# Kernel optimization log

Measured on AMD Instinct MI355X. Metric: run time of the kernel, lower is better.

Reference implementation:

```python
import jax, jax.numpy as jnp
import numpy as np

N_NODES = 50000
N_EDGES = 500000
D_IN = 128
D_HID = 128
OUTPUT_DIM = 10.0


def gcn_conv(x, src, dst, edge_weight, W, b, n_nodes):
    # PyG GCNConv: out = D^{-1/2} (A + I) D^{-1/2} X W + b, self-loop weight 1
    xw = x @ W  # [N, D_out]
    # degree at target nodes, including self-loop weight 1
    deg = jax.ops.segment_sum(edge_weight, dst, num_segments=n_nodes) + 1.0
    dinv = jnp.where(deg > 0, jax.lax.rsqrt(deg), 0.0)  # [N]
    norm = dinv[src] * edge_weight * dinv[dst]  # [E]
    msgs = xw[src] * norm[:, None]  # [E, D_out] gathered+scaled messages
    agg = jax.ops.segment_sum(msgs, dst, num_segments=n_nodes)
    # analytic self-loop contribution: norm_ii = dinv_i * 1 * dinv_i
    agg = agg + xw * (dinv * dinv)[:, None]
    return agg + b


def setup_inputs() -> dict:
    key = jax.random.key(0)
    k = jax.random.split(key, 8)
    x = jax.random.normal(k[0], (N_NODES, D_IN), dtype=jnp.float32)
    edge_index = jax.random.randint(k[1], (2, N_EDGES), 0, N_NODES, dtype=jnp.int64)
    edge_weight = jax.random.uniform(k[2], (N_EDGES,), dtype=jnp.float32)
    s1 = 1.0 / np.sqrt(D_IN)
    s2 = 1.0 / np.sqrt(D_HID)
    W1 = jax.random.uniform(k[3], (D_IN, D_HID), minval=-s1, maxval=s1, dtype=jnp.float32)
    b1 = jnp.zeros((D_HID,), dtype=jnp.float32)
    W2 = jax.random.uniform(k[4], (D_HID, D_HID), minval=-s2, maxval=s2, dtype=jnp.float32)
    b2 = jnp.zeros((D_HID,), dtype=jnp.float32)
    Wf = jax.random.uniform(k[5], (D_HID, 1), minval=-s2, maxval=s2, dtype=jnp.float32)
    bf = jax.random.uniform(k[6], (1,), minval=-s2, maxval=s2, dtype=jnp.float32)
    return {"x": x, "edge_index": edge_index, "edge_weight": edge_weight,
            "W1": W1, "b1": b1, "W2": W2, "b2": b2, "Wf": Wf, "bf": bf}


def reference(x, edge_index, edge_weight, W1, b1, W2, b2, Wf, bf):
    src, dst = edge_index[0], edge_index[1]
    h = gcn_conv(x, src, dst, edge_weight, W1, b1, N_NODES)
    h = gcn_conv(h, src, dst, edge_weight, W2, b2, N_NODES)
    out = h @ Wf + bf  # [N, 1]
    return jax.nn.sigmoid(out) * OUTPUT_DIM
```

## Files before the change

### kernel.cpp

```cpp
#include <hip/hip_runtime.h>

#define N_NODES 50000
#define N_EDGES 500000
#define D 128
#define FXS 4194304.0f
#define CAP 64

typedef unsigned long long u64;
typedef unsigned int uint;

__global__ void init_kernel(const float* __restrict__ W1, const float* __restrict__ W2,
                            const float* __restrict__ b1, const float* __restrict__ b2,
                            const float* __restrict__ Wf, const float* __restrict__ bf,
                            u64* __restrict__ degcnt, float* __restrict__ v,
                            float* __restrict__ consts, int zb) {
    if ((int)blockIdx.x == zb) {
        __shared__ float u[D];
        int t = threadIdx.x;
        if (t < D) {
            float a = 0.f;
#pragma unroll 8
            for (int j = 0; j < D; ++j) a += W2[t * D + j] * Wf[j];
            u[t] = a;
        }
        __syncthreads();
        if (t < D) {
            float a = 0.f;
#pragma unroll 8
            for (int k = 0; k < D; ++k) a += W1[t * D + k] * u[k];
            v[t] = a;
        }
        if (t == 0) {
            float c = 0.f;
            for (int k = 0; k < D; ++k) c += b1[k] * u[k];
            consts[0] = c;
        } else if (t == 1) {
            float c = bf[0];
            for (int k = 0; k < D; ++k) c += b2[k] * Wf[k];
            consts[1] = c;
        }
        return;
    }
    int i = blockIdx.x * 256 + threadIdx.x;
    if (i < N_NODES) degcnt[i] = 0;
}

__global__ void fused_kernel(const int* __restrict__ src, const int* __restrict__ dst,
                             const float* __restrict__ ew, const float* __restrict__ x,
                             const float* __restrict__ v,
                             u64* __restrict__ degcnt, uint* __restrict__ pairs,
                             float* __restrict__ tvec, int eb) {
    int b = blockIdx.x;
    if (b < eb) {
        int e = b * 256 + threadIdx.x;
        if (e < N_EDGES) {
            int d = dst[e];
            float w = ew[e];
            unsigned fx = __float2uint_rn(w * FXS);
            u64 old = atomicAdd(&degcnt[d], (1ull << 32) | (u64)fx);
            int slot = (int)(old >> 32);
            uint pk = ((uint)src[e] << 16) | (uint)__float2uint_rn(w * 65535.0f);
            if (slot < CAP)
                pairs[d * CAP + slot] = pk;
        }
    } else {
        __shared__ float vs[D];
        const int t = threadIdx.x;
        if (t < D) vs[t] = v[t];
        __syncthreads();
        const int lane = t & 63;
        const int n = (b - eb) * 4 + (t >> 6);
        float2 xv = ((const float2*)(x + (size_t)n * D))[lane];
        float a = xv.x * vs[lane * 2] + xv.y * vs[lane * 2 + 1];
#pragma unroll
        for (int off = 32; off > 0; off >>= 1) a += __shfl_xor(a, off);
        if (lane == 0) tvec[n] = a;
    }
}

__global__ void epi_kernel(const u64* __restrict__ degcnt, const float* __restrict__ tvec,
                           float* __restrict__ dinv, float* __restrict__ tw,
                           int* __restrict__ cntv) {
    int n = blockIdx.x * blockDim.x + threadIdx.x;
    if (n < N_NODES) {
        u64 dc = degcnt[n];
        int c = (int)(dc >> 32);
        float deg = (float)(unsigned)(dc & 0xffffffffu) * (1.0f / FXS);
        float di = rsqrtf(deg + 1.0f);
        dinv[n] = di;
        cntv[n] = (c < CAP) ? c : CAP;
        tw[n] = di * tvec[n];
    }
}

__global__ void gather_s_kernel(const float* __restrict__ tw, const float* __restrict__ dinv,
                                const int* __restrict__ cntv, const uint* __restrict__ pairs,
                                const float* __restrict__ consts, float* __restrict__ sw) {
    int tid = threadIdx.x;
    int n = blockIdx.x * 32 + (tid >> 3);
    int l = tid & 7;
    if (n >= N_NODES) return;
    int cnt = cntv[n];
    const uint* row = pairs + (size_t)n * CAP;
    float acc = 0.f;
    for (int i = l; i < cnt; i += 8) {
        uint p = row[i];
        acc += (float)(p & 0xffffu) * (1.0f / 65535.0f) * tw[p >> 16];
    }
    acc += __shfl_xor(acc, 1);
    acc += __shfl_xor(acc, 2);
    acc += __shfl_xor(acc, 4);
    if (l == 0) {
        float di = dinv[n];
        float s = di * (acc + tw[n]) + consts[0];
        sw[n] = di * s;
    }
}

__global__ void gather_z_kernel(const float* __restrict__ sw, const float* __restrict__ dinv,
                                const int* __restrict__ cntv, const uint* __restrict__ pairs,
                                const float* __restrict__ consts, float* __restrict__ out) {
    int tid = threadIdx.x;
    int n = blockIdx.x * 32 + (tid >> 3);
    int l = tid & 7;
    if (n >= N_NODES) return;
    int cnt = cntv[n];
    const uint* row = pairs + (size_t)n * CAP;
    float acc = 0.f;
    for (int i = l; i < cnt; i += 8) {
        uint p = row[i];
        acc += (float)(p & 0xffffu) * (1.0f / 65535.0f) * sw[p >> 16];
    }
    acc += __shfl_xor(acc, 1);
    acc += __shfl_xor(acc, 2);
    acc += __shfl_xor(acc, 4);
    if (l == 0) {
        float di = dinv[n];
        float z = di * (acc + sw[n]) + consts[1];
        out[n] = 10.0f / (1.0f + expf(-z));
    }
}

extern "C" void kernel_launch(void* const* d_in, const int* in_sizes, int n_in,
                              void* d_out, int out_size, void* d_ws, size_t ws_size,
                              hipStream_t stream) {
    const float* x  = (const float*)d_in[0];
    const int*   ei = (const int*)d_in[1];
    const float* ew = (const float*)d_in[2];
    const float* W1 = (const float*)d_in[3];
    const float* b1 = (const float*)d_in[4];
    const float* W2 = (const float*)d_in[5];
    const float* b2 = (const float*)d_in[6];
    const float* Wf = (const float*)d_in[7];
    const float* bf = (const float*)d_in[8];
    const int* srcv = ei;
    const int* dstv = ei + N_EDGES;
    float* out = (float*)d_out;

    char* p = (char*)d_ws;
    auto alloc = [&](size_t bytes) { void* r = (void*)p; p += (bytes + 255) & ~(size_t)255; return r; };
    u64*   degcnt = (u64*)alloc((size_t)N_NODES * 8);
    float* dinv   = (float*)alloc(N_NODES * 4);
    int*   cntv   = (int*)alloc(N_NODES * 4);
    float* tvec   = (float*)alloc(N_NODES * 4);
    float* tw     = (float*)alloc(N_NODES * 4);
    float* sw     = (float*)alloc(N_NODES * 4);
    float* v      = (float*)alloc(D * 4);
    float* consts = (float*)alloc(2 * 4);
    uint*  pairs  = (uint*)alloc((size_t)N_NODES * CAP * 4);

    const int EB = (N_EDGES + 255) / 256;
    const int NB = (N_NODES + 255) / 256;

    init_kernel<<<NB + 1, 256, 0, stream>>>(W1, W2, b1, b2, Wf, bf, degcnt, v, consts, NB);

    fused_kernel<<<EB + N_NODES / 4, 256, 0, stream>>>(srcv, dstv, ew, x, v,
                                                       degcnt, pairs, tvec, EB);

    epi_kernel<<<NB, 256, 0, stream>>>(degcnt, tvec, dinv, tw, cntv);

    gather_s_kernel<<<(N_NODES + 31) / 32, 256, 0, stream>>>(tw, dinv, cntv, pairs, consts, sw);
    gather_z_kernel<<<(N_NODES + 31) / 32, 256, 0, stream>>>(sw, dinv, cntv, pairs, consts, out);
}
```

Before: 139.2 us.

## Merge all stages into one cooperative persistent kernel with grid syncs

Replaces the five separate kernel launches with a single cooperative kernel of 512 blocks that runs each stage in grid-stride loops and separates the stages with grid-wide barriers. This removes per-launch overhead and the gaps between dependent kernels. In exchange, the edge-scatter stage uses only 256 blocks and the node-projection stage the other 256. Grid.sync barriers also cost something, and a fixed grid may underfill the device for the gather stages.

```diff
diff --git a/kernel.cpp b/kernel.cpp
--- a/kernel.cpp
+++ b/kernel.cpp
@@ -1,59 +1,69 @@
 #include <hip/hip_runtime.h>
+#include <hip/hip_cooperative_groups.h>
+
+namespace cg = cooperative_groups;
 
 #define N_NODES 50000
 #define N_EDGES 500000
 #define D 128
 #define FXS 4194304.0f
 #define CAP 64
+#define NBLK 512
+#define NTHR 256
+#define EBLK 256
 
 typedef unsigned long long u64;
 typedef unsigned int uint;
 
-__global__ void init_kernel(const float* __restrict__ W1, const float* __restrict__ W2,
-                            const float* __restrict__ b1, const float* __restrict__ b2,
-                            const float* __restrict__ Wf, const float* __restrict__ bf,
-                            u64* __restrict__ degcnt, float* __restrict__ v,
-                            float* __restrict__ consts, int zb) {
-    if ((int)blockIdx.x == zb) {
-        __shared__ float u[D];
-        int t = threadIdx.x;
-        if (t < D) {
+__global__ __launch_bounds__(NTHR, 4) void mono_kernel(
+    const int* __restrict__ src, const int* __restrict__ dst,
+    const float* __restrict__ ew, const float* __restrict__ x,
+    const float* __restrict__ W1, const float* __restrict__ W2,
+    const float* __restrict__ b1, const float* __restrict__ b2,
+    const float* __restrict__ Wf, const float* __restrict__ bf,
+    u64* __restrict__ degcnt, uint* __restrict__ pairs,
+    float* __restrict__ tvec, float* __restrict__ dinv,
+    int* __restrict__ cntv, float* __restrict__ tw,
+    float* __restrict__ sw, float* __restrict__ v,
+    float* __restrict__ consts, float* __restrict__ out)
+{
+    cg::grid_group grid = cg::this_grid();
+    const int tid = threadIdx.x;
+    const int bid = blockIdx.x;
+    __shared__ float u[D];
+    __shared__ float vs[D];
+
+    if (bid == NBLK - 1) {
+        if (tid < D) {
             float a = 0.f;
 #pragma unroll 8
-            for (int j = 0; j < D; ++j) a += W2[t * D + j] * Wf[j];
-            u[t] = a;
+            for (int j = 0; j < D; ++j) a += W2[tid * D + j] * Wf[j];
+            u[tid] = a;
         }
         __syncthreads();
-        if (t < D) {
+        if (tid < D) {
             float a = 0.f;
 #pragma unroll 8
-            for (int k = 0; k < D; ++k) a += W1[t * D + k] * u[k];
-            v[t] = a;
+            for (int k = 0; k < D; ++k) a += W1[tid * D + k] * u[k];
+            v[tid] = a;
         }
-        if (t == 0) {
+        if (tid == 0) {
             float c = 0.f;
             for (int k = 0; k < D; ++k) c += b1[k] * u[k];
             consts[0] = c;
-        } else if (t == 1) {
+        } else if (tid == 1) {
             float c = bf[0];
             for (int k = 0; k < D; ++k) c += b2[k] * Wf[k];
             consts[1] = c;
         }
-        return;
+    } else {
+        int i = bid * NTHR + tid;
+        if (i < N_NODES) degcnt[i] = 0;
     }
-    int i = blockIdx.x * 256 + threadIdx.x;
-    if (i < N_NODES) degcnt[i] = 0;
-}
+    grid.sync();
 
-__global__ void fused_kernel(const int* __restrict__ src, const int* __restrict__ dst,
-                             const float* __restrict__ ew, const float* __restrict__ x,
-                             const float* __restrict__ v,
-                             u64* __restrict__ degcnt, uint* __restrict__ pairs,
-                             float* __restrict__ tvec, int eb) {
-    int b = blockIdx.x;
-    if (b < eb) {
-        int e = b * 256 + threadIdx.x;
-        if (e < N_EDGES) {
+    if (bid < EBLK) {
+        for (int e = bid * NTHR + tid; e < N_EDGES; e += EBLK * NTHR) {
             int d = dst[e];
             float w = ew[e];
             unsigned fx = __float2uint_rn(w * FXS);
@@ -64,98 +74,96 @@
                 pairs[d * CAP + slot] = pk;
         }
     } else {
-        __shared__ float vs[D];
-        const int t = threadIdx.x;
-        if (t < D) vs[t] = v[t];
+        if (tid < D) vs[tid] = v[tid];
         __syncthreads();
-        const int lane = t & 63;
-        const int n = (b - eb) * 4 + (t >> 6);
-        float2 xv = ((const float2*)(x + (size_t)n * D))[lane];
-        float a = xv.x * vs[lane * 2] + xv.y * vs[lane * 2 + 1];
+        const int lane = tid & 63;
+        const int wv = tid >> 6;
+        for (int n = (bid - EBLK) * 4 + wv; n < N_NODES; n += (NBLK - EBLK) * 4) {
+            float2 xv = ((const float2*)(x + (size_t)n * D))[lane];
+            float a = xv.x * vs[lane * 2] + xv.y * vs[lane * 2 + 1];
 #pragma unroll
-        for (int off = 32; off > 0; off >>= 1) a += __shfl_xor(a, off);
-        if (lane == 0) tvec[n] = a;
+            for (int off = 32; off > 0; off >>= 1) a += __shfl_xor(a, off);
+            if (lane == 0) tvec[n] = a;
+        }
     }
-}
+    grid.sync();
 
-__global__ void epi_kernel(const u64* __restrict__ degcnt, const float* __restrict__ tvec,
-                           float* __restrict__ dinv, float* __restrict__ tw,
-                           int* __restrict__ cntv) {
-    int n = blockIdx.x * blockDim.x + threadIdx.x;
-    if (n < N_NODES) {
-        u64 dc = degcnt[n];
-        int c = (int)(dc >> 32);
-        float deg = (float)(unsigned)(dc & 0xffffffffu) * (1.0f / FXS);
-        float di = rsqrtf(deg + 1.0f);
-        dinv[n] = di;
-        cntv[n] = (c < CAP) ? c : CAP;
-        tw[n] = di * tvec[n];
+    {
+        int n = bid * NTHR + tid;
+        if (n < N_NODES) {
+            u64 dc = degcnt[n];
+            int c = (int)(dc >> 32);
+            float deg = (float)(unsigned)(dc & 0xffffffffu) * (1.0f / FXS);
+            float di = rsqrtf(deg + 1.0f);
+            dinv[n] = di;
+            cntv[n] = (c < CAP) ? c : CAP;
+            tw[n] = di * tvec[n];
+        }
     }
-}
+    grid.sync();
 
-__global__ void gather_s_kernel(const float* __restrict__ tw, const float* __restrict__ dinv,
-                                const int* __restrict__ cntv, const uint* __restrict__ pairs,
-                                const float* __restrict__ consts, float* __restrict__ sw) {
-    int tid = threadIdx.x;
-    int n = blockIdx.x * 32 + (tid >> 3);
-    int l = tid & 7;
-    if (n >= N_NODES) return;
-    int cnt = cntv[n];
-    const uint* row = pairs + (size_t)n * CAP;
-    float acc = 0.f;
-    for (int i = l; i < cnt; i += 8) {
-        uint p = row[i];
-        acc += (float)(p & 0xffffu) * (1.0f / 65535.0f) * tw[p >> 16];
+    const int gid = bid * NTHR + tid;
+    const int l = gid & 7;
+    const int nslot = gid >> 3;
+    for (int base = 0; base < N_NODES; base += (NBLK * NTHR) / 8) {
+        int n = base + nslot;
+        if (n < N_NODES) {
+            int cnt = cntv[n];
+            const uint* row = pairs + (size_t)n * CAP;
+            float acc = 0.f;
+            for (int i = l; i < cnt; i += 8) {
+                uint pk = row[i];
+                acc += (float)(pk & 0xffffu) * (1.0f / 65535.0f) * tw[pk >> 16];
+            }
+            acc += __shfl_xor(acc, 1);
+            acc += __shfl_xor(acc, 2);
+            acc += __shfl_xor(acc, 4);
+            if (l == 0) {
+                float di = dinv[n];
+                float s = di * (acc + tw[n]) + consts[0];
+                sw[n] = di * s;
+            }
+        }
     }
-    acc += __shfl_xor(acc, 1);
-    acc += __shfl_xor(acc, 2);
-    acc += __shfl_xor(acc, 4);
-    if (l == 0) {
-        float di = dinv[n];
-        float s = di * (acc + tw[n]) + consts[0];
-        sw[n] = di * s;
-    }
-}
+    grid.sync();
 
-__global__ void gather_z_kernel(const float* __restrict__ sw, const float* __restrict__ dinv,
-                                const int* __restrict__ cntv, const uint* __restrict__ pairs,
-                                const float* __restrict__ consts, float* __restrict__ out) {
-    int tid = threadIdx.x;
-    int n = blockIdx.x * 32 + (tid >> 3);
-    int l = tid & 7;
-    if (n >= N_NODES) return;
-    int cnt = cntv[n];
-    const uint* row = pairs + (size_t)n * CAP;
-    float acc = 0.f;
-    for (int i = l; i < cnt; i += 8) {
-        uint p = row[i];
-        acc += (float)(p & 0xffffu) * (1.0f / 65535.0f) * sw[p >> 16];
-    }
-    acc += __shfl_xor(acc, 1);
-    acc += __shfl_xor(acc, 2);
-    acc += __shfl_xor(acc, 4);
-    if (l == 0) {
-        float di = dinv[n];
-        float z = di * (acc + sw[n]) + consts[1];
-        out[n] = 10.0f / (1.0f + expf(-z));
+    for (int base = 0; base < N_NODES; base += (NBLK * NTHR) / 8) {
+        int n = base + nslot;
+        if (n < N_NODES) {
+            int cnt = cntv[n];
+            const uint* row = pairs + (size_t)n * CAP;
+            float acc = 0.f;
+            for (int i = l; i < cnt; i += 8) {
+                uint pk = row[i];
+                acc += (float)(pk & 0xffffu) * (1.0f / 65535.0f) * sw[pk >> 16];
+            }
+            acc += __shfl_xor(acc, 1);
+            acc += __shfl_xor(acc, 2);
+            acc += __shfl_xor(acc, 4);
+            if (l == 0) {
+                float di = dinv[n];
+                float z = di * (acc + sw[n]) + consts[1];
+                out[n] = 10.0f / (1.0f + expf(-z));
+            }
+        }
     }
 }
 
 extern "C" void kernel_launch(void* const* d_in, const int* in_sizes, int n_in,
                               void* d_out, int out_size, void* d_ws, size_t ws_size,
                               hipStream_t stream) {
-    const float* x  = (const float*)d_in[0];
     const int*   ei = (const int*)d_in[1];
-    const float* ew = (const float*)d_in[2];
-    const float* W1 = (const float*)d_in[3];
-    const float* b1 = (const float*)d_in[4];
-    const float* W2 = (const float*)d_in[5];
-    const float* b2 = (const float*)d_in[6];
-    const float* Wf = (const float*)d_in[7];
-    const float* bf = (const float*)d_in[8];
     const int* srcv = ei;
     const int* dstv = ei + N_EDGES;
-    float* out = (float*)d_out;
+    const float* xp  = (const float*)d_in[0];
+    const float* ewp = (const float*)d_in[2];
+    const float* W1p = (const float*)d_in[3];
+    const float* b1p = (const float*)d_in[4];
+    const float* W2p = (const float*)d_in[5];
+    const float* b2p = (const float*)d_in[6];
+    const float* Wfp = (const float*)d_in[7];
+    const float* bfp = (const float*)d_in[8];
+    float* outp = (float*)d_out;
 
     char* p = (char*)d_ws;
     auto alloc = [&](size_t bytes) { void* r = (void*)p; p += (bytes + 255) & ~(size_t)255; return r; };
@@ -169,16 +177,14 @@
     float* consts = (float*)alloc(2 * 4);
     uint*  pairs  = (uint*)alloc((size_t)N_NODES * CAP * 4);
 
-    const int EB = (N_EDGES + 255) / 256;
-    const int NB = (N_NODES + 255) / 256;
-
-    init_kernel<<<NB + 1, 256, 0, stream>>>(W1, W2, b1, b2, Wf, bf, degcnt, v, consts, NB);
-
-    fused_kernel<<<EB + N_NODES / 4, 256, 0, stream>>>(srcv, dstv, ew, x, v,
-                                                       degcnt, pairs, tvec, EB);
-
-    epi_kernel<<<NB, 256, 0, stream>>>(degcnt, tvec, dinv, tw, cntv);
-
-    gather_s_kernel<<<(N_NODES + 31) / 32, 256, 0, stream>>>(tw, dinv, cntv, pairs, consts, sw);
-    gather_z_kernel<<<(N_NODES + 31) / 32, 256, 0, stream>>>(sw, dinv, cntv, pairs, consts, out);
+    void* args[] = {
+        (void*)&srcv, (void*)&dstv, (void*)&ewp, (void*)&xp,
+        (void*)&W1p, (void*)&W2p, (void*)&b1p, (void*)&b2p,
+        (void*)&Wfp, (void*)&bfp,
+        (void*)&degcnt, (void*)&pairs, (void*)&tvec, (void*)&dinv,
+        (void*)&cntv, (void*)&tw, (void*)&sw, (void*)&v,
+        (void*)&consts, (void*)&outp
+    };
+    hipLaunchCooperativeKernel((const void*)mono_kernel, dim3(NBLK), dim3(NTHR),
+                               args, 0, stream);
 }
```

After: 374.7 us. 169% more time.
